# Kernel tuning notes

Hardware: AMD Instinct MI355X
Metric: run time of the kernel (lower is better)

Reference implementation:

```python
import jax, jax.numpy as jnp
import numpy as np

N = 100000   # nodes
E = 800000   # directed edges
IN = 256     # in_channels (== hidden, required by repo's vn MLP dims)
HID = 256    # hidden_channels
OUT = 40     # out_channels (arxiv classes)
EPS = 1e-5


def setup_inputs() -> dict:
    key = jax.random.key(0)
    ks = jax.random.split(key, 8)
    def nrm(k, shape, scale=0.05):
        return jax.random.normal(k, shape, dtype=jnp.float32) * scale
    return {
        "x": nrm(ks[0], (N, IN), 1.0),
        "edge_index": jax.random.randint(ks[1], (2, E), 0, N, dtype=jnp.int32),
        # GCNConv weights (PyG: x @ W, then normalized aggregation, then + bias)
        "W0": nrm(ks[2], (IN, HID)),  "b0": jnp.zeros((HID,), jnp.float32),
        "W1": nrm(ks[3], (HID, HID)), "b1": jnp.zeros((HID,), jnp.float32),
        "W2": nrm(ks[4], (HID, OUT)), "b2": jnp.zeros((OUT,), jnp.float32),
        # BatchNorm1d affine params (batch-stat math, training mode)
        "bn_g0": jnp.ones((HID,), jnp.float32), "bn_b0": jnp.zeros((HID,), jnp.float32),
        "bn_g1": jnp.ones((HID,), jnp.float32), "bn_b1": jnp.zeros((HID,), jnp.float32),
        # virtual node embedding (init to 0 per reset_parameters)
        "vn_emb": jnp.zeros((1, IN), jnp.float32),
        # mlp_vns[0]: Linear(IN,HID) + LayerNorm(HID) + ReLU
        "vn_W0": nrm(ks[5], (IN, HID)),  "vn_b0": jnp.zeros((HID,), jnp.float32),
        "ln_g0": jnp.ones((HID,), jnp.float32), "ln_b0": jnp.zeros((HID,), jnp.float32),
        # mlp_vns[1]: Linear(HID,HID) + LayerNorm(HID) + ReLU
        "vn_W1": nrm(ks[6], (HID, HID)), "vn_b1": jnp.zeros((HID,), jnp.float32),
        "ln_g1": jnp.ones((HID,), jnp.float32), "ln_b1": jnp.zeros((HID,), jnp.float32),
    }


def _forward(x, edge_index, W0, b0, W1, b1, W2, b2, bn_g0, bn_b0, bn_g1, bn_b1,
             vn_emb, vn_W0, vn_b0, ln_g0, ln_b0, vn_W1, vn_b1, ln_g1, ln_b1):
    src, dst = edge_index[0], edge_index[1]
    # GCN symmetric normalization with self-loops: deg = in-degree + 1
    deg = jax.ops.segment_sum(jnp.ones(src.shape, jnp.float32), dst, num_segments=N) + 1.0
    dis = jax.lax.rsqrt(deg)                       # deg^{-1/2}  [N]
    coef = (dis[src] * dis[dst])[:, None]          # edge norm   [E,1]
    self_coef = (dis * dis)[:, None]               # self-loop norm = deg^{-1}  [N,1]

    def gcn(h, W, b):
        h = h @ W                                             # [N, out]
        agg = jax.ops.segment_sum(h[src] * coef, dst, num_segments=N)
        return agg + h * self_coef + b

    def bn(h, g, bv):  # BatchNorm1d, batch statistics over nodes
        mu = h.mean(0)
        var = ((h - mu) ** 2).mean(0)
        return (h - mu) * jax.lax.rsqrt(var + EPS) * g + bv

    def ln(h, g, bv):  # LayerNorm over last dim
        mu = h.mean(-1, keepdims=True)
        var = ((h - mu) ** 2).mean(-1, keepdims=True)
        return (h - mu) * jax.lax.rsqrt(var + EPS) * g + bv

    vx = vn_emb                                   # [1, IN]
    # layer 0
    h = x + vx                                    # virtual-node broadcast
    h = gcn(h, W0, b0)
    h = jax.nn.relu(bn(h, bn_g0, bn_b0))          # dropout = identity (eval)
    pool = jnp.sum(h, axis=0, keepdims=True)      # global_add_pool
    vx = jax.nn.relu(ln((pool + vx) @ vn_W0 + vn_b0, ln_g0, ln_b0))
    # layer 1
    h = h + vx
    h = gcn(h, W1, b1)
    h = jax.nn.relu(bn(h, bn_g1, bn_b1))
    pool = jnp.sum(h, axis=0, keepdims=True)
    vx = jax.nn.relu(ln((pool + vx) @ vn_W1 + vn_b1, ln_g1, ln_b1))
    # layer 2 (output)
    h = h + vx
    h = gcn(h, W2, b2)
    return jax.nn.log_softmax(h, axis=-1)


def reference(x, edge_index, W0, b0, W1, b1, W2, b2, bn_g0, bn_b0, bn_g1, bn_b1,
              vn_emb, vn_W0, vn_b0, ln_g0, ln_b0, vn_W1, vn_b1, ln_g1, ln_b1):
    return _forward(x, edge_index, W0, b0, W1, b1, W2, b2, bn_g0, bn_b0, bn_g1, bn_b1,
                    vn_emb, vn_W0, vn_b0, ln_g0, ln_b0, vn_W1, vn_b1, ln_g1, ln_b1)
```

## Files before the change

### kernel.cpp

```cpp
#include <hip/hip_runtime.h>
#include <hip/hip_bf16.h>
#include <cstdint>

#define N_NODES 100000
#define N_EDGES 800000
#define CH      256
#define COUT    40
#define COUTP   48
#define EPS     1e-5f
#define SCAN_CHUNK 1024
#define NSCAN_BLK  98
#define SB_NBLK 500
#define SB_ROWS 200

typedef unsigned short u16;
typedef unsigned int   u32;
typedef short s16x8 __attribute__((ext_vector_type(8)));
typedef float f32x4 __attribute__((ext_vector_type(4)));

__device__ __forceinline__ float b2f(u32 u) { return __uint_as_float(u << 16); }
__device__ __forceinline__ u16 f2b(float f) {
    u32 u = __float_as_uint(f);
    u32 r = (u + 0x7fffu + ((u >> 16) & 1u)) >> 16;
    return (u16)r;
}
__device__ __forceinline__ u32 packb(float a, float b) {
    return (u32)f2b(a) | ((u32)f2b(b) << 16);
}
__device__ __forceinline__ void unpack8(uint4 v, float* f) {
    f[0] = b2f(v.x & 0xffffu); f[1] = b2f(v.x >> 16);
    f[2] = b2f(v.y & 0xffffu); f[3] = b2f(v.y >> 16);
    f[4] = b2f(v.z & 0xffffu); f[5] = b2f(v.z >> 16);
    f[6] = b2f(v.w & 0xffffu); f[7] = b2f(v.w >> 16);
}

__global__ void k_count(const int* __restrict__ dst, int* __restrict__ counts) {
    int e = blockIdx.x * 256 + threadIdx.x;
    if (e < N_EDGES) atomicAdd(&counts[dst[e]], 1);
}

__global__ void k_scan1(const int* __restrict__ counts, int* __restrict__ partial,
                        int* __restrict__ blocksums) {
    __shared__ int sdata[256];
    int base = blockIdx.x * SCAN_CHUNK;
    int t = threadIdx.x;
    int v[4]; int s = 0;
    for (int j = 0; j < 4; j++) {
        int i = base + t * 4 + j;
        v[j] = (i < N_NODES) ? counts[i] : 0;
        s += v[j];
    }
    sdata[t] = s; __syncthreads();
    for (int off = 1; off < 256; off <<= 1) {
        int x = (t >= off) ? sdata[t - off] : 0;
        __syncthreads();
        sdata[t] += x;
        __syncthreads();
    }
    int incl = sdata[t];
    int run = incl - s;
    if (t == 255) blocksums[blockIdx.x] = incl;
    for (int j = 0; j < 4; j++) {
        int i = base + t * 4 + j;
        if (i < N_NODES) partial[i] = run;
        run += v[j];
    }
}

__global__ void k_scan2(int* __restrict__ blocksums) {
    __shared__ int sd[128];
    int t = threadIdx.x;
    int v = (t < NSCAN_BLK) ? blocksums[t] : 0;
    sd[t] = v; __syncthreads();
    for (int off = 1; off < 128; off <<= 1) {
        int x = (t >= off) ? sd[t - off] : 0;
        __syncthreads();
        sd[t] += x;
        __syncthreads();
    }
    if (t < NSCAN_BLK) blocksums[t] = sd[t] - v;
}

__global__ void k_scan3(int* __restrict__ row_start, const int* __restrict__ blocksums,
                        int* __restrict__ cursor, const int* __restrict__ counts,
                        float* __restrict__ dis) {
    int i = blockIdx.x * 256 + threadIdx.x;
    if (i < N_NODES) {
        int v = row_start[i] + blocksums[i >> 10];
        row_start[i] = v;
        cursor[i] = v;
        dis[i] = rsqrtf(1.0f + (float)counts[i]);
    }
}

__global__ void k_fill(const int* __restrict__ src, const int* __restrict__ dst,
                       int* __restrict__ cursor, int* __restrict__ csr,
                       const float* __restrict__ dis, float* __restrict__ coefv) {
    int e = blockIdx.x * 256 + threadIdx.x;
    if (e < N_EDGES) {
        int d = dst[e], s = src[e];
        int p = atomicAdd(&cursor[d], 1);
        csr[p] = s;
        coefv[p] = dis[s] * dis[d];
    }
}

__global__ void k_wt3(const float* __restrict__ W0, const float* __restrict__ W1,
                      const float* __restrict__ W2,
                      u16* __restrict__ T0, u16* __restrict__ T1, u16* __restrict__ T2) {
    int b = blockIdx.x, k = threadIdx.x;
    if (b < 256) {
        T0[b * 256 + k] = f2b(W0[k * 256 + b]);
    } else if (b < 512) {
        int n = b - 256;
        T1[n * 256 + k] = f2b(W1[k * 256 + n]);
    } else {
        int n = b - 512;
        T2[n * 256 + k] = f2b(n < COUT ? W2[k * COUT + n] : 0.f);
    }
}

__global__ void k_vecmat(const float* __restrict__ vec, const float* __restrict__ W,
                         int ncols, int npad, float* __restrict__ outv) {
    __shared__ float s[256];
    int t = threadIdx.x;
    s[t] = vec[t];
    __syncthreads();
    float acc = 0.f;
    if (t < ncols) {
        for (int k = 0; k < 256; k++) acc += s[k] * W[k * ncols + t];
    }
    if (t < npad) outv[t] = acc;
}

__global__ __launch_bounds__(256) void k_gemm(const u16* __restrict__ A,
                                              const u16* __restrict__ Wt,
                                              u16* __restrict__ Hout) {
    __shared__ u16 Bs[256 * 72];
    __shared__ u16 As[64 * 72];
    const int t = threadIdx.x;
    const int wave = t >> 6, lane = t & 63;
    const int lm = lane & 15, quad = lane >> 4;
    const int m0 = blockIdx.x * 64;
    const int ar = t >> 2, as_ = (t & 3) * 16;
    const int arow = m0 + ar;
    const f32x4 vz = {0.f, 0.f, 0.f, 0.f};
    f32x4 acc[4][4];
    for (int m = 0; m < 4; m++)
        for (int c = 0; c < 4; c++) acc[m][c] = vz;

    for (int k0 = 0; k0 < 256; k0 += 64) {
        {
            const uint4* bsrc = (const uint4*)(Wt + t * 256 + k0);
            uint4* bdst = (uint4*)(Bs + t * 72);
#pragma unroll
            for (int j = 0; j < 8; j++) bdst[j] = bsrc[j];
            uint4 a0v = {0,0,0,0}, a1v = {0,0,0,0};
            if (arow < N_NODES) {
                const uint4* asrc = (const uint4*)(A + (size_t)arow * 256 + k0 + as_);
                a0v = asrc[0]; a1v = asrc[1];
            }
            uint4* adst = (uint4*)(As + ar * 72 + as_);
            adst[0] = a0v; adst[1] = a1v;
        }
        __syncthreads();
#pragma unroll
        for (int kk = 0; kk < 64; kk += 32) {
            s16x8 af[4], bf[4];
#pragma unroll
            for (int m = 0; m < 4; m++)
                af[m] = *(const s16x8*)(As + (m * 16 + lm) * 72 + kk + quad * 8);
#pragma unroll
            for (int c = 0; c < 4; c++)
                bf[c] = *(const s16x8*)(Bs + (wave * 64 + c * 16 + lm) * 72 + kk + quad * 8);
#pragma unroll
            for (int c = 0; c < 4; c++)
#pragma unroll
                for (int m = 0; m < 4; m++)
                    acc[m][c] = __builtin_amdgcn_mfma_f32_16x16x32_bf16(af[m], bf[c], acc[m][c], 0, 0, 0);
        }
        __syncthreads();
    }
#pragma unroll
    for (int m = 0; m < 4; m++) {
#pragma unroll
        for (int c = 0; c < 4; c++) {
            int col = wave * 64 + c * 16 + lm;
#pragma unroll
            for (int i = 0; i < 4; i++) {
                int row = m0 + m * 16 + quad * 4 + i;
                if (row < N_NODES) Hout[(size_t)row * 256 + col] = f2b(acc[m][c][i]);
            }
        }
    }
}

__global__ __launch_bounds__(256) void k_gemm_f32a(const float* __restrict__ A,
                                                   const u16* __restrict__ Wt,
                                                   u16* __restrict__ Hout) {
    __shared__ u16 Bs[256 * 72];
    __shared__ u16 As[64 * 72];
    const int t = threadIdx.x;
    const int wave = t >> 6, lane = t & 63;
    const int lm = lane & 15, quad = lane >> 4;
    const int m0 = blockIdx.x * 64;
    const int ar = t >> 2, as_ = (t & 3) * 16;
    const int arow = m0 + ar;
    const f32x4 vz = {0.f, 0.f, 0.f, 0.f};
    f32x4 acc[4][4];
    for (int m = 0; m < 4; m++)
        for (int c = 0; c < 4; c++) acc[m][c] = vz;

    for (int k0 = 0; k0 < 256; k0 += 64) {
        {
            const uint4* bsrc = (const uint4*)(Wt + t * 256 + k0);
            uint4* bdst = (uint4*)(Bs + t * 72);
#pragma unroll
            for (int j = 0; j < 8; j++) bdst[j] = bsrc[j];
            uint4 p0 = {0,0,0,0}, p1 = {0,0,0,0};
            if (arow < N_NODES) {
                const float4* asrc = (const float4*)(A + (size_t)arow * 256 + k0 + as_);
                float4 x0 = asrc[0], x1 = asrc[1], x2 = asrc[2], x3 = asrc[3];
                p0.x = packb(x0.x, x0.y); p0.y = packb(x0.z, x0.w);
                p0.z = packb(x1.x, x1.y); p0.w = packb(x1.z, x1.w);
                p1.x = packb(x2.x, x2.y); p1.y = packb(x2.z, x2.w);
                p1.z = packb(x3.x, x3.y); p1.w = packb(x3.z, x3.w);
            }
            uint4* adst = (uint4*)(As + ar * 72 + as_);
            adst[0] = p0; adst[1] = p1;
        }
        __syncthreads();
#pragma unroll
        for (int kk = 0; kk < 64; kk += 32) {
            s16x8 af[4], bf[4];
#pragma unroll
            for (int m = 0; m < 4; m++)
                af[m] = *(const s16x8*)(As + (m * 16 + lm) * 72 + kk + quad * 8);
#pragma unroll
            for (int c = 0; c < 4; c++)
                bf[c] = *(const s16x8*)(Bs + (wave * 64 + c * 16 + lm) * 72 + kk + quad * 8);
#pragma unroll
            for (int c = 0; c < 4; c++)
#pragma unroll
                for (int m = 0; m < 4; m++)
                    acc[m][c] = __builtin_amdgcn_mfma_f32_16x16x32_bf16(af[m], bf[c], acc[m][c], 0, 0, 0);
        }
        __syncthreads();
    }
#pragma unroll
    for (int m = 0; m < 4; m++) {
#pragma unroll
        for (int c = 0; c < 4; c++) {
            int col = wave * 64 + c * 16 + lm;
#pragma unroll
            for (int i = 0; i < 4; i++) {
                int row = m0 + m * 16 + quad * 4 + i;
                if (row < N_NODES) Hout[(size_t)row * 256 + col] = f2b(acc[m][c][i]);
            }
        }
    }
}

__global__ __launch_bounds__(256) void k_gemm2(const u16* __restrict__ A,
                                               const u16* __restrict__ Wt,
                                               u16* __restrict__ Hout) {
    __shared__ u16 Bs[48 * 72];
    __shared__ u16 As[64 * 72];
    const int t = threadIdx.x;
    const int wave = t >> 6, lane = t & 63;
    const int lm = lane & 15, quad = lane >> 4;
    const int m0 = blockIdx.x * 64;
    const int ar = t >> 2, as_ = (t & 3) * 16;
    const int arow = m0 + ar;
    const f32x4 vz = {0.f, 0.f, 0.f, 0.f};
    f32x4 acc[3]; acc[0] = vz; acc[1] = vz; acc[2] = vz;

    for (int k0 = 0; k0 < 256; k0 += 64) {
        {
            if (t < 48) {
                const uint4* bsrc = (const uint4*)(Wt + t * 256 + k0);
                uint4* bdst = (uint4*)(Bs + t * 72);
#pragma unroll
                for (int j = 0; j < 8; j++) bdst[j] = bsrc[j];
            }
            uint4 a0v = {0,0,0,0}, a1v = {0,0,0,0};
            if (arow < N_NODES) {
                const uint4* asrc = (const uint4*)(A + (size_t)arow * 256 + k0 + as_);
                a0v = asrc[0]; a1v = asrc[1];
            }
            uint4* adst = (uint4*)(As + ar * 72 + as_);
            adst[0] = a0v; adst[1] = a1v;
        }
        __syncthreads();
#pragma unroll
        for (int kk = 0; kk < 64; kk += 32) {
            s16x8 af = *(const s16x8*)(As + (wave * 16 + lm) * 72 + kk + quad * 8);
#pragma unroll
            for (int c = 0; c < 3; c++) {
                s16x8 bf = *(const s16x8*)(Bs + (c * 16 + lm) * 72 + kk + quad * 8);
                acc[c] = __builtin_amdgcn_mfma_f32_16x16x32_bf16(af, bf, acc[c], 0, 0, 0);
            }
        }
        __syncthreads();
    }
#pragma unroll
    for (int c = 0; c < 3; c++) {
        int col = c * 16 + lm;
#pragma unroll
        for (int i = 0; i < 4; i++) {
            int row = m0 + wave * 16 + quad * 4 + i;
            if (row < N_NODES) Hout[(size_t)row * COUTP + col] = f2b(acc[c][i]);
        }
    }
}

__global__ __launch_bounds__(256) void k_agg(const u16* __restrict__ H2,
                                             const int* __restrict__ row_start,
                                             const int* __restrict__ counts,
                                             const int* __restrict__ csr,
                                             const float* __restrict__ coefv,
                                             const float* __restrict__ dis,
                                             const float* __restrict__ bias,
                                             const float* __restrict__ v2,
                                             u16* __restrict__ OutB,
                                             float* __restrict__ stats) {
    __shared__ float ls[512];
    const int t = threadIdx.x, wave = t >> 6, lane = t & 63;
    const int half = lane >> 5, hl = lane & 31;
    const int ci = hl * 8;
    float bb[8], vv[8];
    {
        float4 a = *(const float4*)(bias + ci);
        float4 b = *(const float4*)(bias + ci + 4);
        float4 c = *(const float4*)(v2 + ci);
        float4 d = *(const float4*)(v2 + ci + 4);
        bb[0]=a.x; bb[1]=a.y; bb[2]=a.z; bb[3]=a.w; bb[4]=b.x; bb[5]=b.y; bb[6]=b.z; bb[7]=b.w;
        vv[0]=c.x; vv[1]=c.y; vv[2]=c.z; vv[3]=c.w; vv[4]=d.x; vv[5]=d.y; vv[6]=d.z; vv[7]=d.w;
    }
    float s[8], q[8];
#pragma unroll
    for (int j = 0; j < 8; j++) { s[j] = 0.f; q[j] = 0.f; }
    const int nbase = blockIdx.x * 64 + wave * 16 + half;
    for (int i = 0; i < 16; i += 2) {
        const int node = nbase + i;
        if (node >= N_NODES) break;
        const int beg = row_start[node], cnt = counts[node];
        const float dn = dis[node];
        float a[8];
#pragma unroll
        for (int j = 0; j < 8; j++) a[j] = 0.f;
        float cs = 0.f;
        int e = 0;
        for (; e + 4 <= cnt; e += 4) {
            int ia = csr[beg+e], ib = csr[beg+e+1], ic = csr[beg+e+2], id = csr[beg+e+3];
            float ca = coefv[beg+e], cb = coefv[beg+e+1], cc = coefv[beg+e+2], cd = coefv[beg+e+3];
            uint4 ra = *(const uint4*)(H2 + (size_t)ia * 256 + ci);
            uint4 rb = *(const uint4*)(H2 + (size_t)ib * 256 + ci);
            uint4 rc = *(const uint4*)(H2 + (size_t)ic * 256 + ci);
            uint4 rd = *(const uint4*)(H2 + (size_t)id * 256 + ci);
            cs += ca + cb + cc + cd;
            float fa[8], fb[8], fc[8], fd[8];
            unpack8(ra, fa); unpack8(rb, fb); unpack8(rc, fc); unpack8(rd, fd);
#pragma unroll
            for (int j = 0; j < 8; j++)
                a[j] += ca * fa[j] + cb * fb[j] + cc * fc[j] + cd * fd[j];
        }
        for (; e < cnt; e++) {
            int ia = csr[beg+e]; float ca = coefv[beg+e];
            uint4 ra = *(const uint4*)(H2 + (size_t)ia * 256 + ci);
            cs += ca;
            float fa[8]; unpack8(ra, fa);
#pragma unroll
            for (int j = 0; j < 8; j++) a[j] += ca * fa[j];
        }
        uint4 rs = *(const uint4*)(H2 + (size_t)node * 256 + ci);
        float fs[8]; unpack8(rs, fs);
        const float sc = dn * dn, cv = cs + sc;
        float f[8];
#pragma unroll
        for (int j = 0; j < 8; j++) {
            f[j] = a[j] + sc * fs[j] + cv * vv[j] + bb[j];
            s[j] += f[j]; q[j] += f[j] * f[j];
        }
        uint4 o = {packb(f[0], f[1]), packb(f[2], f[3]), packb(f[4], f[5]), packb(f[6], f[7])};
        *(uint4*)(OutB + (size_t)node * 256 + ci) = o;
    }
    ls[t] = 0.f; ls[256 + t] = 0.f;
    __syncthreads();
#pragma unroll
    for (int j = 0; j < 8; j++) {
        atomicAdd(&ls[ci + j], s[j]);
        atomicAdd(&ls[256 + ci + j], q[j]);
    }
    __syncthreads();
    atomicAdd(&stats[t], ls[t]);
    atomicAdd(&stats[256 + t], ls[256 + t]);
}

__global__ __launch_bounds__(256) void k_bnrelu(const u16* __restrict__ OutB,
                                                const float* __restrict__ stats,
                                                const float* __restrict__ g,
                                                const float* __restrict__ bb_,
                                                u16* __restrict__ Hr,
                                                float* __restrict__ pool) {
    __shared__ float lp[256];
    const int t = threadIdx.x;
    const int cg = (t & 31) * 8;
    const int rg = t >> 5;
    const int r0 = blockIdx.x * SB_ROWS + rg;
    const float inv = 1.0f / (float)N_NODES;
    float gg[8], bc[8];
#pragma unroll
    for (int j = 0; j < 8; j++) {
        int c = cg + j;
        float mu = stats[c] * inv;
        float var = stats[256 + c] * inv - mu * mu;
        float rs = rsqrtf(var + EPS);
        gg[j] = g[c] * rs;
        bc[j] = bb_[c] - mu * gg[j];
    }
    float ps[8];
#pragma unroll
    for (int j = 0; j < 8; j++) ps[j] = 0.f;
#pragma unroll 2
    for (int it = 0; it < SB_ROWS / 8; it++) {
        int r = r0 + it * 8;
        uint4 v = *(const uint4*)(OutB + (size_t)r * 256 + cg);
        float f[8]; unpack8(v, f);
#pragma unroll
        for (int j = 0; j < 8; j++) {
            f[j] = fmaxf(f[j] * gg[j] + bc[j], 0.f);
            ps[j] += f[j];
        }
        uint4 o = {packb(f[0], f[1]), packb(f[2], f[3]), packb(f[4], f[5]), packb(f[6], f[7])};
        *(uint4*)(Hr + (size_t)r * 256 + cg) = o;
    }
    lp[t] = 0.f;
    __syncthreads();
#pragma unroll
    for (int j = 0; j < 8; j++) atomicAdd(&lp[cg + j], ps[j]);
    __syncthreads();
    atomicAdd(&pool[t], lp[t]);
}

__global__ void k_vx(const float* __restrict__ pool, const float* __restrict__ vx_old,
                     const float* __restrict__ vnW, const float* __restrict__ vnb,
                     const float* __restrict__ lng, const float* __restrict__ lnb,
                     float* __restrict__ vx_new,
                     const float* __restrict__ Wnext, int ncn, int npn,
                     float* __restrict__ v2n) {
    __shared__ float s[256];
    __shared__ float red[256];
    int t = threadIdx.x;
    s[t] = pool[t] + vx_old[t];
    __syncthreads();
    float y = vnb[t];
    for (int k = 0; k < 256; k++) y += s[k] * vnW[k * 256 + t];
    red[t] = y; __syncthreads();
    for (int off = 128; off > 0; off >>= 1) {
        if (t < off) red[t] += red[t + off];
        __syncthreads();
    }
    float mu = red[0] * (1.f / 256.f);
    __syncthreads();
    float d = y - mu;
    red[t] = d * d; __syncthreads();
    for (int off = 128; off > 0; off >>= 1) {
        if (t < off) red[t] += red[t + off];
        __syncthreads();
    }
    float var = red[0] * (1.f / 256.f);
    float v = fmaxf(d * rsqrtf(var + EPS) * lng[t] + lnb[t], 0.f);
    vx_new[t] = v;
    __syncthreads();
    s[t] = v;
    __syncthreads();
    float acc = 0.f;
    if (t < ncn) {
        for (int k = 0; k < 256; k++) acc += s[k] * Wnext[k * ncn + t];
    }
    if (t < npn) v2n[t] = acc;
}

__global__ __launch_bounds__(256) void k_agg2(const u16* __restrict__ H2,
                                              const int* __restrict__ row_start,
                                              const int* __restrict__ counts,
                                              const int* __restrict__ csr,
                                              const float* __restrict__ coefv,
                                              const float* __restrict__ dis,
                                              const float* __restrict__ bias,
                                              const float* __restrict__ v2,
                                              float* __restrict__ OutF) {
    const int t = threadIdx.x, wave = t >> 6, lane = t & 63;
    const int half = lane >> 5, hl = lane & 31;
    const bool gact = hl < 24;
    const bool cact = hl < 20;
    const int c0 = 2 * hl;
    float bb0 = 0.f, bb1 = 0.f, vv0 = 0.f, vv1 = 0.f;
    if (cact) {
        float2 bv = *(const float2*)(bias + c0); bb0 = bv.x; bb1 = bv.y;
        float2 vvv = *(const float2*)(v2 + c0);  vv0 = vvv.x; vv1 = vvv.y;
    }
    const int nbase = blockIdx.x * 16 + wave * 4;
    for (int i = 0; i < 4; i++) {
        const int node = nbase + i;
        const int beg = row_start[node], cnt = counts[node];
        const float dn = dis[node];
        float a0 = 0.f, a1 = 0.f, cs = 0.f;
        int e = half;
        for (; e + 6 < cnt; e += 8) {
            int ia = csr[beg+e], ib = csr[beg+e+2], ic = csr[beg+e+4], id = csr[beg+e+6];
            float ca = coefv[beg+e], cb = coefv[beg+e+2], cc = coefv[beg+e+4], cd = coefv[beg+e+6];
            u32 ra = 0, rb = 0, rc = 0, rd = 0;
            if (gact) {
                ra = *(const u32*)(H2 + (size_t)ia * COUTP + c0);
                rb = *(const u32*)(H2 + (size_t)ib * COUTP + c0);
                rc = *(const u32*)(H2 + (size_t)ic * COUTP + c0);
                rd = *(const u32*)(H2 + (size_t)id * COUTP + c0);
            }
            cs += ca + cb + cc + cd;
            a0 += ca*b2f(ra&0xffffu) + cb*b2f(rb&0xffffu) + cc*b2f(rc&0xffffu) + cd*b2f(rd&0xffffu);
            a1 += ca*b2f(ra>>16)     + cb*b2f(rb>>16)     + cc*b2f(rc>>16)     + cd*b2f(rd>>16);
        }
        for (; e < cnt; e += 2) {
            int ia = csr[beg+e]; float ca = coefv[beg+e];
            u32 ra = gact ? *(const u32*)(H2 + (size_t)ia * COUTP + c0) : 0u;
            cs += ca;
            a0 += ca*b2f(ra&0xffffu); a1 += ca*b2f(ra>>16);
        }
        a0 += __shfl_xor(a0, 32);
        a1 += __shfl_xor(a1, 32);
        cs += __shfl_xor(cs, 32);
        const float sc = dn * dn;
        u32 rs_ = gact ? *(const u32*)(H2 + (size_t)node * COUTP + c0) : 0u;
        float h0 = a0 + sc*b2f(rs_&0xffffu) + (cs+sc)*vv0 + bb0;
        float h1 = a1 + sc*b2f(rs_>>16)     + (cs+sc)*vv1 + bb1;
        float m = cact ? fmaxf(h0, h1) : -3.0e38f;
#pragma unroll
        for (int off = 16; off > 0; off >>= 1) m = fmaxf(m, __shfl_xor(m, off));
        float ex = cact ? (expf(h0 - m) + expf(h1 - m)) : 0.f;
        float se = ex;
#pragma unroll
        for (int off = 16; off > 0; off >>= 1) se += __shfl_xor(se, off);
        float lg = logf(se);
        if (cact && half == 0) {
            float2 o = {h0 - m - lg, h1 - m - lg};
            *(float2*)(OutF + (size_t)node * COUT + c0) = o;
        }
    }
}

extern "C" void kernel_launch(void* const* d_in, const int* in_sizes, int n_in,
                              void* d_out, int out_size, void* d_ws, size_t ws_size,
                              hipStream_t stream) {
    const float* x   = (const float*)d_in[0];
    const int*   ei  = (const int*)d_in[1];
    const int*   esrc = ei;
    const int*   edst = ei + N_EDGES;
    const float* W0 = (const float*)d_in[2];  const float* b0 = (const float*)d_in[3];
    const float* W1 = (const float*)d_in[4];  const float* b1 = (const float*)d_in[5];
    const float* W2 = (const float*)d_in[6];  const float* b2 = (const float*)d_in[7];
    const float* bg0 = (const float*)d_in[8]; const float* bb0 = (const float*)d_in[9];
    const float* bg1 = (const float*)d_in[10]; const float* bb1 = (const float*)d_in[11];
    const float* vn_emb = (const float*)d_in[12];
    const float* vW0 = (const float*)d_in[13]; const float* vb0 = (const float*)d_in[14];
    const float* lg0 = (const float*)d_in[15]; const float* lb0 = (const float*)d_in[16];
    const float* vW1 = (const float*)d_in[17]; const float* vb1 = (const float*)d_in[18];
    const float* lg1 = (const float*)d_in[19]; const float* lb1 = (const float*)d_in[20];

    char* w = (char*)d_ws;
    auto alloc = [&](size_t bytes) { void* p = (void*)w; w += ((bytes + 255) / 256) * 256; return p; };
    u16* H2    = (u16*)alloc((size_t)N_NODES * 256 * 2);
    u16* HR    = (u16*)alloc((size_t)N_NODES * 256 * 2);
    u16* OutB  = (u16*)alloc((size_t)N_NODES * 256 * 2);
    int* csr   = (int*)alloc((size_t)N_EDGES * 4);
    float* coefv = (float*)alloc((size_t)N_EDGES * 4);
    int* counts = (int*)alloc((size_t)N_NODES * 4);
    int* rowst  = (int*)alloc((size_t)N_NODES * 4);
    int* cursor = (int*)alloc((size_t)N_NODES * 4);
    float* dis  = (float*)alloc((size_t)N_NODES * 4);
    u16* Wtb0 = (u16*)alloc(256 * 256 * 2);
    u16* Wtb1 = (u16*)alloc(256 * 256 * 2);
    u16* Wt2b = (u16*)alloc(COUTP * 256 * 2);
    int* scanblk = (int*)alloc(128 * 4);
    float* stats = (float*)alloc(768 * 4);
    float* vxA = (float*)alloc(256 * 4);
    float* vxB = (float*)alloc(256 * 4);
    float* v20 = (float*)alloc(256 * 4);
    float* v21 = (float*)alloc(256 * 4);
    float* v22 = (float*)alloc(64 * 4);
    (void)ws_size; (void)in_sizes; (void)n_in; (void)out_size; (void)vxB;

    hipMemsetAsync(counts, 0, (size_t)N_NODES * 4, stream);
    k_count<<<(N_EDGES + 255) / 256, 256, 0, stream>>>(edst, counts);
    k_scan1<<<NSCAN_BLK, 256, 0, stream>>>(counts, rowst, scanblk);
    k_scan2<<<1, 128, 0, stream>>>(scanblk);
    k_scan3<<<(N_NODES + 255) / 256, 256, 0, stream>>>(rowst, scanblk, cursor, counts, dis);
    k_fill<<<(N_EDGES + 255) / 256, 256, 0, stream>>>(esrc, edst, cursor, csr, dis, coefv);

    k_wt3<<<512 + COUTP, 256, 0, stream>>>(W0, W1, W2, Wtb0, Wtb1, Wt2b);
    k_vecmat<<<1, 256, 0, stream>>>(vn_emb, W0, 256, 256, v20);

    const int aggblk = (N_NODES + 63) / 64;

    k_gemm_f32a<<<(N_NODES + 63) / 64, 256, 0, stream>>>(x, Wtb0, H2);
    hipMemsetAsync(stats, 0, 768 * 4, stream);
    k_agg<<<aggblk, 256, 0, stream>>>(H2, rowst, counts, csr, coefv, dis, b0, v20, OutB, stats);
    k_bnrelu<<<SB_NBLK, 256, 0, stream>>>(OutB, stats, bg0, bb0, HR, stats + 512);
    k_vx<<<1, 256, 0, stream>>>(stats + 512, vn_emb, vW0, vb0, lg0, lb0, vxA, W1, 256, 256, v21);

    k_gemm<<<(N_NODES + 63) / 64, 256, 0, stream>>>(HR, Wtb1, H2);
    hipMemsetAsync(stats, 0, 768 * 4, stream);
    k_agg<<<aggblk, 256, 0, stream>>>(H2, rowst, counts, csr, coefv, dis, b1, v21, OutB, stats);
    k_bnrelu<<<SB_NBLK, 256, 0, stream>>>(OutB, stats, bg1, bb1, HR, stats + 512);
    k_vx<<<1, 256, 0, stream>>>(stats + 512, vxA, vW1, vb1, lg1, lb1, vxB, W2, COUT, COUTP, v22);

    k_gemm2<<<(N_NODES + 63) / 64, 256, 0, stream>>>(HR, Wt2b, H2);
    k_agg2<<<N_NODES / 16, 256, 0, stream>>>(H2, rowst, counts, csr, coefv, dis, b2, v22, (float*)d_out);
}
```

Before: 779.1 us.

## Fuse BatchNorm+ReLU+pooling into next GEMM prologue and pack edge data

Removes the standalone BN/ReLU kernel by applying the normalization, ReLU and the global-add-pool partial sums inside the A-tile load of the following GEMM. This drops one full read and write of the activation matrix per layer. Pool sums are spread over 8 slots to reduce atomic contention, and k_vx reduces those slots. The CSR source index and edge coefficient are packed into one int2 array, and the aggregation kernel is reshaped so each wave handles 16 nodes with 4 channels per lane instead of 8. The cost is extra shuffle and LDS-atomic work in the GEMM prologue, plus BN math recomputed per block.

```diff
diff --git a/kernel.cpp b/kernel.cpp
--- a/kernel.cpp
+++ b/kernel.cpp
@@ -10,8 +10,7 @@
 #define EPS     1e-5f
 #define SCAN_CHUNK 1024
 #define NSCAN_BLK  98
-#define SB_NBLK 500
-#define SB_ROWS 200
+#define AGG_NPW 16
 
 typedef unsigned short u16;
 typedef unsigned int   u32;
@@ -94,14 +93,14 @@
 }
 
 __global__ void k_fill(const int* __restrict__ src, const int* __restrict__ dst,
-                       int* __restrict__ cursor, int* __restrict__ csr,
-                       const float* __restrict__ dis, float* __restrict__ coefv) {
+                       int* __restrict__ cursor, int2* __restrict__ edata,
+                       const float* __restrict__ dis) {
     int e = blockIdx.x * 256 + threadIdx.x;
     if (e < N_EDGES) {
         int d = dst[e], s = src[e];
         int p = atomicAdd(&cursor[d], 1);
-        csr[p] = s;
-        coefv[p] = dis[s] * dis[d];
+        int2 v; v.x = s; v.y = __float_as_int(dis[s] * dis[d]);
+        edata[p] = v;
     }
 }
 
@@ -131,68 +130,6 @@
         for (int k = 0; k < 256; k++) acc += s[k] * W[k * ncols + t];
     }
     if (t < npad) outv[t] = acc;
-}
-
-__global__ __launch_bounds__(256) void k_gemm(const u16* __restrict__ A,
-                                              const u16* __restrict__ Wt,
-                                              u16* __restrict__ Hout) {
-    __shared__ u16 Bs[256 * 72];
-    __shared__ u16 As[64 * 72];
-    const int t = threadIdx.x;
-    const int wave = t >> 6, lane = t & 63;
-    const int lm = lane & 15, quad = lane >> 4;
-    const int m0 = blockIdx.x * 64;
-    const int ar = t >> 2, as_ = (t & 3) * 16;
-    const int arow = m0 + ar;
-    const f32x4 vz = {0.f, 0.f, 0.f, 0.f};
-    f32x4 acc[4][4];
-    for (int m = 0; m < 4; m++)
-        for (int c = 0; c < 4; c++) acc[m][c] = vz;
-
-    for (int k0 = 0; k0 < 256; k0 += 64) {
-        {
-            const uint4* bsrc = (const uint4*)(Wt + t * 256 + k0);
-            uint4* bdst = (uint4*)(Bs + t * 72);
-#pragma unroll
-            for (int j = 0; j < 8; j++) bdst[j] = bsrc[j];
-            uint4 a0v = {0,0,0,0}, a1v = {0,0,0,0};
-            if (arow < N_NODES) {
-                const uint4* asrc = (const uint4*)(A + (size_t)arow * 256 + k0 + as_);
-                a0v = asrc[0]; a1v = asrc[1];
-            }
-            uint4* adst = (uint4*)(As + ar * 72 + as_);
-            adst[0] = a0v; adst[1] = a1v;
-        }
-        __syncthreads();
-#pragma unroll
-        for (int kk = 0; kk < 64; kk += 32) {
-            s16x8 af[4], bf[4];
-#pragma unroll
-            for (int m = 0; m < 4; m++)
-                af[m] = *(const s16x8*)(As + (m * 16 + lm) * 72 + kk + quad * 8);
-#pragma unroll
-            for (int c = 0; c < 4; c++)
-                bf[c] = *(const s16x8*)(Bs + (wave * 64 + c * 16 + lm) * 72 + kk + quad * 8);
-#pragma unroll
-            for (int c = 0; c < 4; c++)
-#pragma unroll
-                for (int m = 0; m < 4; m++)
-                    acc[m][c] = __builtin_amdgcn_mfma_f32_16x16x32_bf16(af[m], bf[c], acc[m][c], 0, 0, 0);
-        }
-        __syncthreads();
-    }
-#pragma unroll
-    for (int m = 0; m < 4; m++) {
-#pragma unroll
-        for (int c = 0; c < 4; c++) {
-            int col = wave * 64 + c * 16 + lm;
-#pragma unroll
-            for (int i = 0; i < 4; i++) {
-                int row = m0 + m * 16 + quad * 4 + i;
-                if (row < N_NODES) Hout[(size_t)row * 256 + col] = f2b(acc[m][c][i]);
-            }
-        }
-    }
 }
 
 __global__ __launch_bounds__(256) void k_gemm_f32a(const float* __restrict__ A,
@@ -261,17 +198,131 @@
     }
 }
 
-__global__ __launch_bounds__(256) void k_gemm2(const u16* __restrict__ A,
-                                               const u16* __restrict__ Wt,
-                                               u16* __restrict__ Hout) {
-    __shared__ u16 Bs[48 * 72];
+__global__ __launch_bounds__(256) void k_gemm_bn(const u16* __restrict__ A,
+                                                 const float* __restrict__ stats,
+                                                 const float* __restrict__ g,
+                                                 const float* __restrict__ bv,
+                                                 const u16* __restrict__ Wt,
+                                                 u16* __restrict__ Hout,
+                                                 float* __restrict__ pool) {
+    __shared__ u16 Bs[256 * 72];
     __shared__ u16 As[64 * 72];
+    __shared__ float ggs[256], bcs[256], pls[256];
     const int t = threadIdx.x;
     const int wave = t >> 6, lane = t & 63;
     const int lm = lane & 15, quad = lane >> 4;
     const int m0 = blockIdx.x * 64;
     const int ar = t >> 2, as_ = (t & 3) * 16;
     const int arow = m0 + ar;
+    {
+        const float inv = 1.0f / (float)N_NODES;
+        float mu = stats[t] * inv;
+        float var = stats[256 + t] * inv - mu * mu;
+        float rs = rsqrtf(var + EPS);
+        float gg = g[t] * rs;
+        ggs[t] = gg; bcs[t] = bv[t] - mu * gg;
+        pls[t] = 0.f;
+    }
+    __syncthreads();
+    const f32x4 vz = {0.f, 0.f, 0.f, 0.f};
+    f32x4 acc[4][4];
+    for (int m = 0; m < 4; m++)
+        for (int c = 0; c < 4; c++) acc[m][c] = vz;
+
+    for (int k0 = 0; k0 < 256; k0 += 64) {
+        {
+            const uint4* bsrc = (const uint4*)(Wt + t * 256 + k0);
+            uint4* bdst = (uint4*)(Bs + t * 72);
+#pragma unroll
+            for (int j = 0; j < 8; j++) bdst[j] = bsrc[j];
+            float f[16];
+            if (arow < N_NODES) {
+                const uint4* asrc = (const uint4*)(A + (size_t)arow * 256 + k0 + as_);
+                uint4 r0 = asrc[0], r1 = asrc[1];
+                unpack8(r0, f); unpack8(r1, f + 8);
+#pragma unroll
+                for (int j = 0; j < 16; j++) {
+                    int c = k0 + as_ + j;
+                    f[j] = fmaxf(f[j] * ggs[c] + bcs[c], 0.f);
+                }
+            } else {
+#pragma unroll
+                for (int j = 0; j < 16; j++) f[j] = 0.f;
+            }
+#pragma unroll
+            for (int j = 0; j < 16; j++) {
+                float v = f[j];
+                v += __shfl_xor(v, 4);  v += __shfl_xor(v, 8);
+                v += __shfl_xor(v, 16); v += __shfl_xor(v, 32);
+                if (lane < 4) atomicAdd(&pls[k0 + lane * 16 + j], v);
+            }
+            uint4 p0, p1;
+            p0.x = packb(f[0], f[1]);   p0.y = packb(f[2], f[3]);
+            p0.z = packb(f[4], f[5]);   p0.w = packb(f[6], f[7]);
+            p1.x = packb(f[8], f[9]);   p1.y = packb(f[10], f[11]);
+            p1.z = packb(f[12], f[13]); p1.w = packb(f[14], f[15]);
+            uint4* adst = (uint4*)(As + ar * 72 + as_);
+            adst[0] = p0; adst[1] = p1;
+        }
+        __syncthreads();
+#pragma unroll
+        for (int kk = 0; kk < 64; kk += 32) {
+            s16x8 af[4], bf[4];
+#pragma unroll
+            for (int m = 0; m < 4; m++)
+                af[m] = *(const s16x8*)(As + (m * 16 + lm) * 72 + kk + quad * 8);
+#pragma unroll
+            for (int c = 0; c < 4; c++)
+                bf[c] = *(const s16x8*)(Bs + (wave * 64 + c * 16 + lm) * 72 + kk + quad * 8);
+#pragma unroll
+            for (int c = 0; c < 4; c++)
+#pragma unroll
+                for (int m = 0; m < 4; m++)
+                    acc[m][c] = __builtin_amdgcn_mfma_f32_16x16x32_bf16(af[m], bf[c], acc[m][c], 0, 0, 0);
+        }
+        __syncthreads();
+    }
+    atomicAdd(&pool[(blockIdx.x & 7) * 256 + t], pls[t]);
+#pragma unroll
+    for (int m = 0; m < 4; m++) {
+#pragma unroll
+        for (int c = 0; c < 4; c++) {
+            int col = wave * 64 + c * 16 + lm;
+#pragma unroll
+            for (int i = 0; i < 4; i++) {
+                int row = m0 + m * 16 + quad * 4 + i;
+                if (row < N_NODES) Hout[(size_t)row * 256 + col] = f2b(acc[m][c][i]);
+            }
+        }
+    }
+}
+
+__global__ __launch_bounds__(256) void k_gemm2_bn(const u16* __restrict__ A,
+                                                  const float* __restrict__ stats,
+                                                  const float* __restrict__ g,
+                                                  const float* __restrict__ bv,
+                                                  const u16* __restrict__ Wt,
+                                                  u16* __restrict__ Hout,
+                                                  float* __restrict__ pool) {
+    __shared__ u16 Bs[48 * 72];
+    __shared__ u16 As[64 * 72];
+    __shared__ float ggs[256], bcs[256], pls[256];
+    const int t = threadIdx.x;
+    const int wave = t >> 6, lane = t & 63;
+    const int lm = lane & 15, quad = lane >> 4;
+    const int m0 = blockIdx.x * 64;
+    const int ar = t >> 2, as_ = (t & 3) * 16;
+    const int arow = m0 + ar;
+    {
+        const float inv = 1.0f / (float)N_NODES;
+        float mu = stats[t] * inv;
+        float var = stats[256 + t] * inv - mu * mu;
+        float rs = rsqrtf(var + EPS);
+        float gg = g[t] * rs;
+        ggs[t] = gg; bcs[t] = bv[t] - mu * gg;
+        pls[t] = 0.f;
+    }
+    __syncthreads();
     const f32x4 vz = {0.f, 0.f, 0.f, 0.f};
     f32x4 acc[3]; acc[0] = vz; acc[1] = vz; acc[2] = vz;
 
@@ -283,13 +334,34 @@
 #pragma unroll
                 for (int j = 0; j < 8; j++) bdst[j] = bsrc[j];
             }
-            uint4 a0v = {0,0,0,0}, a1v = {0,0,0,0};
+            float f[16];
             if (arow < N_NODES) {
                 const uint4* asrc = (const uint4*)(A + (size_t)arow * 256 + k0 + as_);
-                a0v = asrc[0]; a1v = asrc[1];
-            }
+                uint4 r0 = asrc[0], r1 = asrc[1];
+                unpack8(r0, f); unpack8(r1, f + 8);
+#pragma unroll
+                for (int j = 0; j < 16; j++) {
+                    int c = k0 + as_ + j;
+                    f[j] = fmaxf(f[j] * ggs[c] + bcs[c], 0.f);
+                }
+            } else {
+#pragma unroll
+                for (int j = 0; j < 16; j++) f[j] = 0.f;
+            }
+#pragma unroll
+            for (int j = 0; j < 16; j++) {
+                float v = f[j];
+                v += __shfl_xor(v, 4);  v += __shfl_xor(v, 8);
+                v += __shfl_xor(v, 16); v += __shfl_xor(v, 32);
+                if (lane < 4) atomicAdd(&pls[k0 + lane * 16 + j], v);
+            }
+            uint4 p0, p1;
+            p0.x = packb(f[0], f[1]);   p0.y = packb(f[2], f[3]);
+            p0.z = packb(f[4], f[5]);   p0.w = packb(f[6], f[7]);
+            p1.x = packb(f[8], f[9]);   p1.y = packb(f[10], f[11]);
+            p1.z = packb(f[12], f[13]); p1.w = packb(f[14], f[15]);
             uint4* adst = (uint4*)(As + ar * 72 + as_);
-            adst[0] = a0v; adst[1] = a1v;
+            adst[0] = p0; adst[1] = p1;
         }
         __syncthreads();
 #pragma unroll
@@ -303,6 +375,7 @@
         }
         __syncthreads();
     }
+    atomicAdd(&pool[(blockIdx.x & 7) * 256 + t], pls[t]);
 #pragma unroll
     for (int c = 0; c < 3; c++) {
         int col = c * 16 + lm;
@@ -317,130 +390,68 @@
 __global__ __launch_bounds__(256) void k_agg(const u16* __restrict__ H2,
                                              const int* __restrict__ row_start,
                                              const int* __restrict__ counts,
-                                             const int* __restrict__ csr,
-                                             const float* __restrict__ coefv,
+                                             const int2* __restrict__ edata,
                                              const float* __restrict__ dis,
                                              const float* __restrict__ bias,
                                              const float* __restrict__ v2,
                                              u16* __restrict__ OutB,
                                              float* __restrict__ stats) {
     __shared__ float ls[512];
-    const int t = threadIdx.x, wave = t >> 6, lane = t & 63;
-    const int half = lane >> 5, hl = lane & 31;
-    const int ci = hl * 8;
-    float bb[8], vv[8];
-    {
-        float4 a = *(const float4*)(bias + ci);
-        float4 b = *(const float4*)(bias + ci + 4);
-        float4 c = *(const float4*)(v2 + ci);
-        float4 d = *(const float4*)(v2 + ci + 4);
-        bb[0]=a.x; bb[1]=a.y; bb[2]=a.z; bb[3]=a.w; bb[4]=b.x; bb[5]=b.y; bb[6]=b.z; bb[7]=b.w;
-        vv[0]=c.x; vv[1]=c.y; vv[2]=c.z; vv[3]=c.w; vv[4]=d.x; vv[5]=d.y; vv[6]=d.z; vv[7]=d.w;
-    }
-    float s[8], q[8];
-#pragma unroll
-    for (int j = 0; j < 8; j++) { s[j] = 0.f; q[j] = 0.f; }
-    const int nbase = blockIdx.x * 64 + wave * 16 + half;
-    for (int i = 0; i < 16; i += 2) {
+    const int t = threadIdx.x, wave = t >> 6, lane = t & 63, ci = lane * 4;
+    const float4 bb = *(const float4*)(bias + ci);
+    const float4 vv = *(const float4*)(v2 + ci);
+    float s0=0,s1=0,s2=0,s3=0,q0=0,q1=0,q2=0,q3=0;
+    const int nbase = blockIdx.x * (4 * AGG_NPW) + wave * AGG_NPW;
+    for (int i = 0; i < AGG_NPW; i++) {
         const int node = nbase + i;
         if (node >= N_NODES) break;
         const int beg = row_start[node], cnt = counts[node];
         const float dn = dis[node];
-        float a[8];
-#pragma unroll
-        for (int j = 0; j < 8; j++) a[j] = 0.f;
-        float cs = 0.f;
+        float a0=0,a1=0,a2=0,a3=0, cs=0;
         int e = 0;
         for (; e + 4 <= cnt; e += 4) {
-            int ia = csr[beg+e], ib = csr[beg+e+1], ic = csr[beg+e+2], id = csr[beg+e+3];
-            float ca = coefv[beg+e], cb = coefv[beg+e+1], cc = coefv[beg+e+2], cd = coefv[beg+e+3];
-            uint4 ra = *(const uint4*)(H2 + (size_t)ia * 256 + ci);
-            uint4 rb = *(const uint4*)(H2 + (size_t)ib * 256 + ci);
-            uint4 rc = *(const uint4*)(H2 + (size_t)ic * 256 + ci);
-            uint4 rd = *(const uint4*)(H2 + (size_t)id * 256 + ci);
+            int2 ea = edata[beg+e],   eb = edata[beg+e+1];
+            int2 ec = edata[beg+e+2], ed = edata[beg+e+3];
+            float ca = __int_as_float(ea.y), cb = __int_as_float(eb.y);
+            float cc = __int_as_float(ec.y), cd = __int_as_float(ed.y);
+            uint2 ra = *(const uint2*)(H2 + (size_t)ea.x * 256 + ci);
+            uint2 rb = *(const uint2*)(H2 + (size_t)eb.x * 256 + ci);
+            uint2 rc = *(const uint2*)(H2 + (size_t)ec.x * 256 + ci);
+            uint2 rd = *(const uint2*)(H2 + (size_t)ed.x * 256 + ci);
             cs += ca + cb + cc + cd;
-            float fa[8], fb[8], fc[8], fd[8];
-            unpack8(ra, fa); unpack8(rb, fb); unpack8(rc, fc); unpack8(rd, fd);
-#pragma unroll
-            for (int j = 0; j < 8; j++)
-                a[j] += ca * fa[j] + cb * fb[j] + cc * fc[j] + cd * fd[j];
+            a0 += ca*b2f(ra.x&0xffffu) + cb*b2f(rb.x&0xffffu) + cc*b2f(rc.x&0xffffu) + cd*b2f(rd.x&0xffffu);
+            a1 += ca*b2f(ra.x>>16)     + cb*b2f(rb.x>>16)     + cc*b2f(rc.x>>16)     + cd*b2f(rd.x>>16);
+            a2 += ca*b2f(ra.y&0xffffu) + cb*b2f(rb.y&0xffffu) + cc*b2f(rc.y&0xffffu) + cd*b2f(rd.y&0xffffu);
+            a3 += ca*b2f(ra.y>>16)     + cb*b2f(rb.y>>16)     + cc*b2f(rc.y>>16)     + cd*b2f(rd.y>>16);
         }
         for (; e < cnt; e++) {
-            int ia = csr[beg+e]; float ca = coefv[beg+e];
-            uint4 ra = *(const uint4*)(H2 + (size_t)ia * 256 + ci);
+            int2 ea = edata[beg+e];
+            float ca = __int_as_float(ea.y);
+            uint2 ra = *(const uint2*)(H2 + (size_t)ea.x * 256 + ci);
             cs += ca;
-            float fa[8]; unpack8(ra, fa);
-#pragma unroll
-            for (int j = 0; j < 8; j++) a[j] += ca * fa[j];
-        }
-        uint4 rs = *(const uint4*)(H2 + (size_t)node * 256 + ci);
-        float fs[8]; unpack8(rs, fs);
+            a0 += ca*b2f(ra.x&0xffffu); a1 += ca*b2f(ra.x>>16);
+            a2 += ca*b2f(ra.y&0xffffu); a3 += ca*b2f(ra.y>>16);
+        }
+        uint2 rs = *(const uint2*)(H2 + (size_t)node * 256 + ci);
         const float sc = dn * dn, cv = cs + sc;
-        float f[8];
-#pragma unroll
-        for (int j = 0; j < 8; j++) {
-            f[j] = a[j] + sc * fs[j] + cv * vv[j] + bb[j];
-            s[j] += f[j]; q[j] += f[j] * f[j];
-        }
-        uint4 o = {packb(f[0], f[1]), packb(f[2], f[3]), packb(f[4], f[5]), packb(f[6], f[7])};
-        *(uint4*)(OutB + (size_t)node * 256 + ci) = o;
+        float f0 = a0 + sc*b2f(rs.x&0xffffu) + cv*vv.x + bb.x;
+        float f1 = a1 + sc*b2f(rs.x>>16)     + cv*vv.y + bb.y;
+        float f2 = a2 + sc*b2f(rs.y&0xffffu) + cv*vv.z + bb.z;
+        float f3 = a3 + sc*b2f(rs.y>>16)     + cv*vv.w + bb.w;
+        uint2 o; o.x = packb(f0, f1); o.y = packb(f2, f3);
+        *(uint2*)(OutB + (size_t)node * 256 + ci) = o;
+        s0 += f0; q0 += f0*f0; s1 += f1; q1 += f1*f1;
+        s2 += f2; q2 += f2*f2; s3 += f3; q3 += f3*f3;
     }
     ls[t] = 0.f; ls[256 + t] = 0.f;
     __syncthreads();
-#pragma unroll
-    for (int j = 0; j < 8; j++) {
-        atomicAdd(&ls[ci + j], s[j]);
-        atomicAdd(&ls[256 + ci + j], q[j]);
-    }
+    atomicAdd(&ls[ci], s0);   atomicAdd(&ls[ci+1], s1);
+    atomicAdd(&ls[ci+2], s2); atomicAdd(&ls[ci+3], s3);
+    atomicAdd(&ls[256+ci], q0);   atomicAdd(&ls[256+ci+1], q1);
+    atomicAdd(&ls[256+ci+2], q2); atomicAdd(&ls[256+ci+3], q3);
     __syncthreads();
     atomicAdd(&stats[t], ls[t]);
     atomicAdd(&stats[256 + t], ls[256 + t]);
-}
-
-__global__ __launch_bounds__(256) void k_bnrelu(const u16* __restrict__ OutB,
-                                                const float* __restrict__ stats,
-                                                const float* __restrict__ g,
-                                                const float* __restrict__ bb_,
-                                                u16* __restrict__ Hr,
-                                                float* __restrict__ pool) {
-    __shared__ float lp[256];
-    const int t = threadIdx.x;
-    const int cg = (t & 31) * 8;
-    const int rg = t >> 5;
-    const int r0 = blockIdx.x * SB_ROWS + rg;
-    const float inv = 1.0f / (float)N_NODES;
-    float gg[8], bc[8];
-#pragma unroll
-    for (int j = 0; j < 8; j++) {
-        int c = cg + j;
-        float mu = stats[c] * inv;
-        float var = stats[256 + c] * inv - mu * mu;
-        float rs = rsqrtf(var + EPS);
-        gg[j] = g[c] * rs;
-        bc[j] = bb_[c] - mu * gg[j];
-    }
-    float ps[8];
-#pragma unroll
-    for (int j = 0; j < 8; j++) ps[j] = 0.f;
-#pragma unroll 2
-    for (int it = 0; it < SB_ROWS / 8; it++) {
-        int r = r0 + it * 8;
-        uint4 v = *(const uint4*)(OutB + (size_t)r * 256 + cg);
-        float f[8]; unpack8(v, f);
-#pragma unroll
-        for (int j = 0; j < 8; j++) {
-            f[j] = fmaxf(f[j] * gg[j] + bc[j], 0.f);
-            ps[j] += f[j];
-        }
-        uint4 o = {packb(f[0], f[1]), packb(f[2], f[3]), packb(f[4], f[5]), packb(f[6], f[7])};
-        *(uint4*)(Hr + (size_t)r * 256 + cg) = o;
-    }
-    lp[t] = 0.f;
-    __syncthreads();
-#pragma unroll
-    for (int j = 0; j < 8; j++) atomicAdd(&lp[cg + j], ps[j]);
-    __syncthreads();
-    atomicAdd(&pool[t], lp[t]);
 }
 
 __global__ void k_vx(const float* __restrict__ pool, const float* __restrict__ vx_old,
@@ -452,7 +463,10 @@
     __shared__ float s[256];
     __shared__ float red[256];
     int t = threadIdx.x;
-    s[t] = pool[t] + vx_old[t];
+    float pv = 0.f;
+#pragma unroll
+    for (int r = 0; r < 8; r++) pv += pool[r * 256 + t];
+    s[t] = pv + vx_old[t];
     __syncthreads();
     float y = vnb[t];
     for (int k = 0; k < 256; k++) y += s[k] * vnW[k * 256 + t];
@@ -485,8 +499,7 @@
 __global__ __launch_bounds__(256) void k_agg2(const u16* __restrict__ H2,
                                               const int* __restrict__ row_start,
                                               const int* __restrict__ counts,
-                                              const int* __restrict__ csr,
-                                              const float* __restrict__ coefv,
+                                              const int2* __restrict__ edata,
                                               const float* __restrict__ dis,
                                               const float* __restrict__ bias,
                                               const float* __restrict__ v2,
@@ -509,22 +522,25 @@
         float a0 = 0.f, a1 = 0.f, cs = 0.f;
         int e = half;
         for (; e + 6 < cnt; e += 8) {
-            int ia = csr[beg+e], ib = csr[beg+e+2], ic = csr[beg+e+4], id = csr[beg+e+6];
-            float ca = coefv[beg+e], cb = coefv[beg+e+2], cc = coefv[beg+e+4], cd = coefv[beg+e+6];
+            int2 ea = edata[beg+e],   eb = edata[beg+e+2];
+            int2 ec = edata[beg+e+4], ed = edata[beg+e+6];
+            float ca = __int_as_float(ea.y), cb = __int_as_float(eb.y);
+            float cc = __int_as_float(ec.y), cd = __int_as_float(ed.y);
             u32 ra = 0, rb = 0, rc = 0, rd = 0;
             if (gact) {
-                ra = *(const u32*)(H2 + (size_t)ia * COUTP + c0);
-                rb = *(const u32*)(H2 + (size_t)ib * COUTP + c0);
-                rc = *(const u32*)(H2 + (size_t)ic * COUTP + c0);
-                rd = *(const u32*)(H2 + (size_t)id * COUTP + c0);
+                ra = *(const u32*)(H2 + (size_t)ea.x * COUTP + c0);
+                rb = *(const u32*)(H2 + (size_t)eb.x * COUTP + c0);
+                rc = *(const u32*)(H2 + (size_t)ec.x * COUTP + c0);
+                rd = *(const u32*)(H2 + (size_t)ed.x * COUTP + c0);
             }
             cs += ca + cb + cc + cd;
             a0 += ca*b2f(ra&0xffffu) + cb*b2f(rb&0xffffu) + cc*b2f(rc&0xffffu) + cd*b2f(rd&0xffffu);
             a1 += ca*b2f(ra>>16)     + cb*b2f(rb>>16)     + cc*b2f(rc>>16)     + cd*b2f(rd>>16);
         }
         for (; e < cnt; e += 2) {
-            int ia = csr[beg+e]; float ca = coefv[beg+e];
-            u32 ra = gact ? *(const u32*)(H2 + (size_t)ia * COUTP + c0) : 0u;
+            int2 ea = edata[beg+e];
+            float ca = __int_as_float(ea.y);
+            u32 ra = gact ? *(const u32*)(H2 + (size_t)ea.x * COUTP + c0) : 0u;
             cs += ca;
             a0 += ca*b2f(ra&0xffffu); a1 += ca*b2f(ra>>16);
         }
@@ -571,10 +587,8 @@
     char* w = (char*)d_ws;
     auto alloc = [&](size_t bytes) { void* p = (void*)w; w += ((bytes + 255) / 256) * 256; return p; };
     u16* H2    = (u16*)alloc((size_t)N_NODES * 256 * 2);
-    u16* HR    = (u16*)alloc((size_t)N_NODES * 256 * 2);
     u16* OutB  = (u16*)alloc((size_t)N_NODES * 256 * 2);
-    int* csr   = (int*)alloc((size_t)N_EDGES * 4);
-    float* coefv = (float*)alloc((size_t)N_EDGES * 4);
+    int2* edata = (int2*)alloc((size_t)N_EDGES * 8);
     int* counts = (int*)alloc((size_t)N_NODES * 4);
     int* rowst  = (int*)alloc((size_t)N_NODES * 4);
     int* cursor = (int*)alloc((size_t)N_NODES * 4);
@@ -583,38 +597,36 @@
     u16* Wtb1 = (u16*)alloc(256 * 256 * 2);
     u16* Wt2b = (u16*)alloc(COUTP * 256 * 2);
     int* scanblk = (int*)alloc(128 * 4);
-    float* stats = (float*)alloc(768 * 4);
+    float* statsA = (float*)alloc(2560 * 4);
+    float* statsB = (float*)alloc(2560 * 4);
     float* vxA = (float*)alloc(256 * 4);
     float* vxB = (float*)alloc(256 * 4);
     float* v20 = (float*)alloc(256 * 4);
     float* v21 = (float*)alloc(256 * 4);
     float* v22 = (float*)alloc(64 * 4);
-    (void)ws_size; (void)in_sizes; (void)n_in; (void)out_size; (void)vxB;
+    (void)ws_size; (void)in_sizes; (void)n_in; (void)out_size;
 
     hipMemsetAsync(counts, 0, (size_t)N_NODES * 4, stream);
+    hipMemsetAsync(statsA, 0, 2560 * 4, stream);
+    hipMemsetAsync(statsB, 0, 2560 * 4, stream);
     k_count<<<(N_EDGES + 255) / 256, 256, 0, stream>>>(edst, counts);
     k_scan1<<<NSCAN_BLK, 256, 0, stream>>>(counts, rowst, scanblk);
     k_scan2<<<1, 128, 0, stream>>>(scanblk);
     k_scan3<<<(N_NODES + 255) / 256, 256, 0, stream>>>(rowst, scanblk, cursor, counts, dis);
-    k_fill<<<(N_EDGES + 255) / 256, 256, 0, stream>>>(esrc, edst, cursor, csr, dis, coefv);
+    k_fill<<<(N_EDGES + 255) / 256, 256, 0, stream>>>(esrc, edst, cursor, edata, dis);
 
     k_wt3<<<512 + COUTP, 256, 0, stream>>>(W0, W1, W2, Wtb0, Wtb1, Wt2b);
     k_vecmat<<<1, 256, 0, stream>>>(vn_emb, W0, 256, 256, v20);
 
+    const int gemmblk = (N_NODES + 63) / 64;
     const int aggblk = (N_NODES + 63) / 64;
 
-    k_gemm_f32a<<<(N_NODES + 63) / 64, 256, 0, stream>>>(x, Wtb0, H2);
-    hipMemsetAsync(stats, 0, 768 * 4, stream);
-    k_agg<<<aggblk, 256, 0, stream>>>(H2, rowst, counts, csr, coefv, dis, b0, v20, OutB, stats);
-    k_bnrelu<<<SB_NBLK, 256, 0, stream>>>(OutB, stats, bg0, bb0, HR, stats + 512);
-    k_vx<<<1, 256, 0, stream>>>(stats + 512, vn_emb, vW0, vb0, lg0, lb0, vxA, W1, 256, 256, v21);
-
-    k_gemm<<<(N_NODES + 63) / 64, 256, 0, stream>>>(HR, Wtb1, H2);
-    hipMemsetAsync(stats, 0, 768 * 4, stream);
-    k_agg<<<aggblk, 256, 0, stream>>>(H2, rowst, counts, csr, coefv, dis, b1, v21, OutB, stats);
-    k_bnrelu<<<SB_NBLK, 256, 0, stream>>>(OutB, stats, bg1, bb1, HR, stats + 512);
-    k_vx<<<1, 256, 0, stream>>>(stats + 512, vxA, vW1, vb1, lg1, lb1, vxB, W2, COUT, COUTP, v22);
-
-    k_gemm2<<<(N_NODES + 63) / 64, 256, 0, stream>>>(HR, Wt2b, H2);
-    k_agg2<<<N_NODES / 16, 256, 0, stream>>>(H2, rowst, counts, csr, coefv, dis, b2, v22, (float*)d_out);
-}
+    k_gemm_f32a<<<gemmblk, 256, 0, stream>>>(x, Wtb0, H2);
+    k_agg<<<aggblk, 256, 0, stream>>>(H2, rowst, counts, edata, dis, b0, v20, OutB, statsA);
+    k_gemm_bn<<<gemmblk, 256, 0, stream>>>(OutB, statsA, bg0, bb0, Wtb1, H2, statsA + 512);
+    k_vx<<<1, 256, 0, stream>>>(statsA + 512, vn_emb, vW0, vb0, lg0, lb0, vxA, W1, 256, 256, v21);
+    k_agg<<<aggblk, 256, 0, stream>>>(H2, rowst, counts, edata, dis, b1, v21, OutB, statsB);
+    k_gemm2_bn<<<gemmblk, 256, 0, stream>>>(OutB, statsB, bg1, bb1, Wt2b, H2, statsB + 512);
+    k_vx<<<1, 256, 0, stream>>>(statsB + 512, vxA, vW1, vb1, lg1, lb1, vxB, W2, COUT, COUTP, v22);
+    k_agg2<<<N_NODES / 16, 256, 0, stream>>>(H2, rowst, counts, edata, dis, b2, v22, (float*)d_out);
+}
```

Result: faster. 753.2 us (-3.3%).
